# Optimization experiments

Hardware: AMD Instinct MI355X
Metric: run time of the kernel (lower is better)

Reference implementation:

```python
import jax, jax.numpy as jnp
import numpy as np

B, N, D = 64, 197, 768
H, HD = 12, 64
MAX_REL = 14
SCALE = HD ** -0.5


def rel_indices(n, max_rel):
    """Static 2D relative-position index matrices of shape (n, n), int32."""
    lq = n - 1
    side = int(lq ** 0.5)
    r = np.arange(lq)
    dv = r[None, :] // side - r[:, None] // side
    dh = r[None, :] % side - r[:, None] % side
    fv = np.clip(dv, -max_rel, max_rel) + max_rel + 1
    fh = np.clip(dh, -max_rel, max_rel) + max_rel + 1
    # pad one row/col of zeros on top-left for the cls token (index 0)
    fv = np.pad(fv, ((1, 0), (1, 0)), constant_values=0)
    fh = np.pad(fh, ((1, 0), (1, 0)), constant_values=0)
    return fv.astype(np.int32), fh.astype(np.int32)


IDX_V, IDX_H = rel_indices(N, MAX_REL)


def setup_inputs() -> dict:
    key = jax.random.key(0)
    ks = jax.random.split(key, 13)
    lin = lambda k: jax.random.normal(k, (D, H * HD), jnp.float32) * 0.02
    tab = lambda k: jax.random.normal(k, (2 * MAX_REL + 2, HD), jnp.float32) * 0.02
    return {
        'x': jax.random.normal(ks[0], (B, N, D), jnp.float32),
        'wq': lin(ks[1]), 'bq': jnp.zeros((H * HD,), jnp.float32),
        'wk': lin(ks[2]), 'bk': jnp.zeros((H * HD,), jnp.float32),
        'wv': lin(ks[3]), 'bv': jnp.zeros((H * HD,), jnp.float32),
        'wp': jax.random.normal(ks[4], (H * HD, D), jnp.float32) * 0.02,
        'bp': jnp.zeros((D,), jnp.float32),
        'rel_k_v': tab(ks[5]), 'rel_k_h': tab(ks[6]),
        'rel_v_v': tab(ks[7]), 'rel_v_h': tab(ks[8]),
    }


def reference(x, wq, bq, wk, bk, wv, bv, wp, bp, rel_k_v, rel_k_h, rel_v_v, rel_v_h):
    b, n, _ = x.shape
    # qkv projections -> (B, H, N, HD)
    q = (x @ wq + bq).reshape(b, n, H, HD).transpose(0, 2, 1, 3)
    k = (x @ wk + bk).reshape(b, n, H, HD).transpose(0, 2, 1, 3)
    v = (x @ wv + bv).reshape(b, n, H, HD).transpose(0, 2, 1, 3)

    attn = jnp.einsum('bhid,bhjd->bhij', q, k) * SCALE
    # iRPE key bias: gather (N, N, HD) table then contract with q per query pos
    r_p_k = rel_k_v[IDX_V] + rel_k_h[IDX_H]              # (N, N, HD)
    attn = attn + jnp.einsum('bhid,ijd->bhij', q, r_p_k) * SCALE
    attn = jax.nn.softmax(attn, axis=-1)

    out = jnp.einsum('bhij,bhjd->bhid', attn, v)
    # iRPE value bias
    r_p_v = rel_v_v[IDX_V] + rel_v_h[IDX_H]              # (N, N, HD)
    out = out + jnp.einsum('bhij,ijd->bhid', attn, r_p_v)

    out = out.transpose(0, 2, 1, 3).reshape(b, n, H * HD)
    return out @ wp + bp
```

## Files before the change

kernel.cpp:

```cpp
#include <hip/hip_runtime.h>
#include <math.h>

#define SCALE_ 0.125f

typedef unsigned short u16;
typedef __attribute__((ext_vector_type(8))) _Float16 half8;
typedef __attribute__((ext_vector_type(4))) float f32x4;
#define MFMA_H __builtin_amdgcn_mfma_f32_16x16x32_f16

__device__ __forceinline__ u16 f2h(float f) {
    union { _Float16 h; u16 u; } v; v.h = (_Float16)f; return v.u;
}
__device__ __forceinline__ float h2f(u16 u) {
    union { _Float16 h; u16 u; } v; v.u = u; return (float)v.h;
}
__device__ __forceinline__ void gload16(const u16* g, u16* l) {
    __builtin_amdgcn_global_load_lds(
        (const __attribute__((address_space(1))) void*)g,
        (__attribute__((address_space(3))) void*)l, 16, 0, 0);
}
__device__ __forceinline__ half8 ld_h8(const u16* p) {
    return *(const half8*)p;
}

__global__ void prep_half_x(const float* __restrict__ x, u16* __restrict__ xh) {
    size_t idx = ((size_t)blockIdx.x * 256 + threadIdx.x) * 8;
    float4 a = *(const float4*)(x + idx), b = *(const float4*)(x + idx + 4);
    float f[8] = {a.x, a.y, a.z, a.w, b.x, b.y, b.z, b.w};
    u16 hs[8];
    #pragma unroll
    for (int e = 0; e < 8; ++e) hs[e] = f2h(f[e]);
    *(uint4*)(xh + idx) = *(uint4*)hs;
}

__global__ void prep_w(const float* __restrict__ w0, const float* __restrict__ w1,
                       const float* __restrict__ w2, const float* __restrict__ w3,
                       u16* o0, u16* o1, u16* o2, u16* o3) {
    const float* W; u16* oh;
    if (blockIdx.z == 0)      { W = w0; oh = o0; }
    else if (blockIdx.z == 1) { W = w1; oh = o1; }
    else if (blockIdx.z == 2) { W = w2; oh = o2; }
    else                      { W = w3; oh = o3; }

    __shared__ float t[64 * 68];
    int k0 = blockIdx.y * 64, n0 = blockIdx.x * 64;
    int tid = threadIdx.x;
    #pragma unroll
    for (int rr = 0; rr < 4; ++rr) {
        int r = (tid >> 4) + rr * 16;
        int c = (tid & 15) * 4;
        *(float4*)&t[r * 68 + c] = *(const float4*)(W + (size_t)(k0 + r) * 768 + n0 + c);
    }
    __syncthreads();
    int n = tid >> 2, kc = (tid & 3) * 16;
    u16 hs[16];
    #pragma unroll
    for (int e = 0; e < 16; ++e) hs[e] = f2h(t[(kc + e) * 68 + n]);
    size_t o = (size_t)(n0 + n) * 768 + k0 + kc;
    *(uint4*)(oh + o) = *(uint4*)hs;
    *(uint4*)(oh + o + 8) = *(uint4*)(hs + 8);
}

__global__ void prep_tabs(const float* __restrict__ rkv, const float* __restrict__ rkh,
                          const float* __restrict__ rvv, const float* __restrict__ rvh,
                          u16* tk, u16* rth) {
    for (int idx = threadIdx.x; idx < 4096; idx += 256) {
        int r = idx >> 6, d = idx & 63;
        float tv = 0.f;
        if (r < 30) tv = rkv[r * 64 + d];
        else if (r >= 32 && r < 62) tv = rkh[(r - 32) * 64 + d];
        tk[idx] = f2h(tv);
        int dd = idx >> 6, rr = idx & 63;
        float vv = 0.f;
        if (rr < 30) vv = rvv[rr * 64 + dd];
        else if (rr >= 32 && rr < 62) vv = rvh[(rr - 32) * 64 + dd];
        rth[idx] = f2h(vv);
    }
}

__global__ void prep_vt(const u16* __restrict__ rth, u16* __restrict__ vtp) {
    u16* vb = vtp + (size_t)blockIdx.x * 64 * 288;
    for (int t = threadIdx.x; t < 64 * 91; t += 256) {
        int d = t / 91;
        int c = 197 + (t - d * 91);
        u16 val = 0;
        if (c >= 208 && c < 272) val = rth[d * 64 + (c - 208)];
        vb[d * 288 + c] = val;
    }
}

__global__ __launch_bounds__(256) void vtrans(const u16* __restrict__ v,
                                              u16* __restrict__ vt) {
    __shared__ u16 L[64 * 72];
    const int bh = blockIdx.x;
    const u16* src = v + (size_t)bh * 197 * 64;
    u16* dst = vt + (size_t)bh * 64 * 288;
    const int tid = threadIdx.x;
    const int keyl = tid >> 2;
    const int c8 = (tid & 3) * 16;
    for (int k0 = 0; k0 < 197; k0 += 64) {
        __syncthreads();
        int key = k0 + keyl;
        if (key < 197) {
            uint4 g0 = *(const uint4*)(src + key * 64 + c8);
            uint4 g1 = *(const uint4*)(src + key * 64 + c8 + 8);
            u16 t0[8]; *(uint4*)t0 = g0;
            u16 t1[8]; *(uint4*)t1 = g1;
            #pragma unroll
            for (int e = 0; e < 8; ++e) L[(c8 + e) * 72 + keyl] = t0[e];
            #pragma unroll
            for (int e = 0; e < 8; ++e) L[(c8 + 8 + e) * 72 + keyl] = t1[e];
        }
        __syncthreads();
        int d = tid >> 2, cc = (tid & 3) * 16;
        if (k0 + cc < 197) {
            int nvalid = min(16, 197 - k0 - cc);
            if (nvalid == 16) {
                *(uint4*)(dst + d * 288 + k0 + cc)     = *(const uint4*)&L[d * 72 + cc];
                *(uint4*)(dst + d * 288 + k0 + cc + 8) = *(const uint4*)&L[d * 72 + cc + 8];
            } else {
                for (int e = 0; e < nvalid; ++e)
                    dst[d * 288 + k0 + cc + e] = L[d * 72 + cc + e];
            }
        }
    }
}

__global__ __launch_bounds__(256, 4) void gemm_f16(
    const u16* __restrict__ Ah,
    const u16* __restrict__ B0, const u16* __restrict__ B1, const u16* __restrict__ B2,
    const float* __restrict__ bias0, const float* __restrict__ bias1,
    const float* __restrict__ bias2,
    u16* qo, u16* ko, u16* vo, float* outf, int nz, int kind)
{
    __shared__ u16 SM[128 * 64 * 2];
    u16* As = SM;
    u16* Bs = SM + 128 * 64;

    const int p = blockIdx.x;
    const int xcd = p & 7, s = p >> 3;
    const int mcnt = (xcd < 3) ? 13 : 12;
    const int mbase = (xcd < 3) ? xcd * 13 : 39 + (xcd - 3) * 12;
    const int jn = 6 * nz;
    if (s >= mcnt * jn) return;
    const int mb = mbase + s / jn;
    const int j = s % jn;
    const int z = j / 6;
    const int nb = j % 6;

    const u16* Bt = B0; const float* bias = bias0;
    if (z == 1) { Bt = B1; bias = bias1; }
    else if (z == 2) { Bt = B2; bias = bias2; }

    const int m0 = mb * 128, n0 = nb * 128;
    const int tid = threadIdx.x;
    const int w = tid >> 6, lane = tid & 63, quad = lane >> 4, l16 = lane & 15;
    const int wm = (w >> 1) * 64, wn = (w & 1) * 64;
    const int rl8 = lane >> 3, cs = lane & 7;
    const int csrc = (cs ^ rl8) * 8;

    f32x4 acc[4][4];
    #pragma unroll
    for (int a = 0; a < 4; ++a)
        #pragma unroll
        for (int b = 0; b < 4; ++b) acc[a][b] = (f32x4){0, 0, 0, 0};

    for (int kt = 0; kt < 768; kt += 64) {
        __syncthreads();
        #pragma unroll
        for (int i = 0; i < 4; ++i) {
            int r = w * 32 + i * 8 + rl8;
            int arow = min(m0 + r, 12607);
            gload16(Ah + (size_t)arow * 768 + kt + csrc, &As[(w * 32 + i * 8) * 64]);
            gload16(Bt + (size_t)(n0 + r) * 768 + kt + csrc, &Bs[(w * 32 + i * 8) * 64]);
        }
        __syncthreads();
        #pragma unroll
        for (int kb = 0; kb < 2; ++kb) {
            const int slot = ((kb * 4 + quad) ^ (l16 & 7)) * 8;
            half8 ah[4], bf[4];
            #pragma unroll
            for (int mi = 0; mi < 4; ++mi) {
                ah[mi] = ld_h8(&As[(wm + mi * 16 + l16) * 64 + slot]);
                bf[mi] = ld_h8(&Bs[(wn + mi * 16 + l16) * 64 + slot]);
            }
            #pragma unroll
            for (int ni = 0; ni < 4; ++ni)
                #pragma unroll
                for (int mi = 0; mi < 4; ++mi)
                    acc[mi][ni] = MFMA_H(ah[mi], bf[ni], acc[mi][ni], 0, 0, 0);
        }
    }

    if (kind == 1) {
        #pragma unroll
        for (int mi = 0; mi < 4; ++mi) {
            #pragma unroll
            for (int r = 0; r < 4; ++r) {
                int gr = m0 + wm + mi * 16 + quad * 4 + r;
                if (gr >= 12608) continue;
                #pragma unroll
                for (int ni = 0; ni < 4; ++ni) {
                    int gc = n0 + wn + ni * 16 + l16;
                    outf[(size_t)gr * 768 + gc] = acc[mi][ni][r] + bias[gc];
                }
            }
        }
        return;
    }

    __syncthreads();
    u16* Cs = SM;
    #pragma unroll
    for (int mi = 0; mi < 4; ++mi) {
        #pragma unroll
        for (int ni = 0; ni < 4; ++ni) {
            int col = wn + ni * 16 + l16;
            float bv = bias[n0 + col];
            #pragma unroll
            for (int r = 0; r < 4; ++r)
                Cs[(wm + mi * 16 + quad * 4 + r) * 128 + col] = f2h(acc[mi][ni][r] + bv);
        }
    }
    __syncthreads();
    u16* O = (z == 0) ? qo : ((z == 1) ? ko : vo);
    int row = tid >> 1, halfc = tid & 1;
    int gr = m0 + row;
    if (gr < 12608) {
        int bb = gr / 197, ii = gr - bb * 197;
        int h = (n0 >> 6) + halfc;
        u16* dst = O + ((size_t)(bb * 12 + h) * 197 + ii) * 64;
        const u16* src = &Cs[row * 128 + halfc * 64];
        #pragma unroll
        for (int e = 0; e < 8; ++e)
            *(uint4*)(dst + e * 8) = *(const uint4*)(src + e * 8);
    }
}

__global__ __launch_bounds__(512, 4) void attn_mfma(
    const u16* __restrict__ qh, const u16* __restrict__ kh,
    const u16* __restrict__ tk, const u16* __restrict__ vt,
    u16* __restrict__ oh)
{
    __shared__ u16 Ph[64 * 296];
    __shared__ float Tvh[64 * 68];
    __shared__ float red[64 * 4];

    const int p = blockIdx.x;
    const int xcd = p & 7, s = p >> 3;
    const int bh = xcd * 96 + (s >> 2);
    const int qt = s & 3;
    const int I0 = qt * 64;
    const int tid = threadIdx.x;
    const int w = tid >> 6, lane = tid & 63, quad = lane >> 4, l16 = lane & 15;
    const int mf = w >> 1, nh = w & 1;
    const int mr0 = mf * 16;
    const size_t base = (size_t)bh * 197 * 64;
    const uint4 z4 = make_uint4(0, 0, 0, 0);

    half8 qa[2];
    {
        int i = I0 + mr0 + l16;
        bool ok = i < 197;
        const u16* qp = qh + base + (size_t)i * 64 + quad * 8;
        #pragma unroll
        for (int kb = 0; kb < 2; ++kb) {
            uint4 a = ok ? *(const uint4*)(qp + kb * 32) : z4;
            *(uint4*)&qa[kb] = a;
        }
    }

    #pragma unroll
    for (int s2 = 0; s2 < 2; ++s2) {
        int c = (nh * 2 + s2) * 16 + l16;
        f32x4 acc = (f32x4){0, 0, 0, 0};
        #pragma unroll
        for (int kb = 0; kb < 2; ++kb) {
            half8 th = ld_h8(tk + c * 64 + kb * 32 + quad * 8);
            acc = MFMA_H(qa[kb], th, acc, 0, 0, 0);
        }
        #pragma unroll
        for (int r = 0; r < 4; ++r)
            Tvh[(mr0 + quad * 4 + r) * 68 + c] = acc[r];
    }

    f32x4 sacc[7];
    #pragma unroll
    for (int s1 = 0; s1 < 7; ++s1) sacc[s1] = (f32x4){0, 0, 0, 0};
    #pragma unroll
    for (int s1 = 0; s1 < 7; ++s1) {
        int j = (nh * 7 + s1) * 16 + l16;
        bool ok = j < 197;
        const u16* kp = kh + base + (size_t)j * 64 + quad * 8;
        f32x4 c = sacc[s1];
        #pragma unroll
        for (int kb = 0; kb < 2; ++kb) {
            uint4 a = ok ? *(const uint4*)(kp + kb * 32) : z4;
            half8 kf; *(uint4*)&kf = a;
            c = MFMA_H(qa[kb], kf, c, 0, 0, 0);
        }
        sacc[s1] = c;
    }
    __syncthreads();

    float sval[7][4];
    int jj[7];
    #pragma unroll
    for (int s1 = 0; s1 < 7; ++s1) jj[s1] = (nh * 7 + s1) * 16 + l16;
    int ivA[4], ihA[4], iA[4];
    #pragma unroll
    for (int r = 0; r < 4; ++r) {
        int i = I0 + mr0 + quad * 4 + r;
        int qi = i - 1;
        int iv = qi / 14;
        ivA[r] = iv; ihA[r] = qi - iv * 14; iA[r] = i;
    }
    #pragma unroll
    for (int s1 = 0; s1 < 7; ++s1) {
        int j = jj[s1];
        if (j < 197) {
            int kj = j - 1;
            int jv = kj / 14;
            int jh2 = kj - jv * 14;
            #pragma unroll
            for (int r = 0; r < 4; ++r) {
                int m = mr0 + quad * 4 + r;
                int fv = 0, fh = 0;
                if (iA[r] > 0 && j > 0) {
                    int dv = jv - ivA[r]; dv = min(14, max(-14, dv));
                    int dh = jh2 - ihA[r]; dh = min(14, max(-14, dh));
                    fv = dv + 15; fh = dh + 15;
                }
                sval[s1][r] = (sacc[s1][r] + Tvh[m * 68 + fv] + Tvh[m * 68 + 32 + fh]) * SCALE_;
            }
        } else {
            #pragma unroll
            for (int r = 0; r < 4; ++r) sval[s1][r] = -1e30f;
        }
    }

    #pragma unroll
    for (int r = 0; r < 4; ++r) {
        float mx = sval[0][r];
        #pragma unroll
        for (int s1 = 1; s1 < 7; ++s1) mx = fmaxf(mx, sval[s1][r]);
        #pragma unroll
        for (int off = 1; off < 16; off <<= 1) mx = fmaxf(mx, __shfl_xor(mx, off, 64));
        if (l16 == 0) red[(mr0 + quad * 4 + r) * 4 + nh] = mx;
    }
    __syncthreads();

    #pragma unroll
    for (int r = 0; r < 4; ++r) {
        int m = mr0 + quad * 4 + r;
        float M = fmaxf(red[m * 4], red[m * 4 + 1]);
        float sum = 0.f;
        #pragma unroll
        for (int s1 = 0; s1 < 7; ++s1) {
            float pv = (jj[s1] < 197) ? __expf(sval[s1][r] - M) : 0.f;
            sval[s1][r] = pv;
            sum += pv;
        }
        #pragma unroll
        for (int off = 1; off < 16; off <<= 1) sum += __shfl_xor(sum, off, 64);
        if (l16 == 0) red[m * 4 + 2 + nh] = sum;
    }
    #pragma unroll
    for (int s1 = 0; s1 < 7; ++s1) {
        int j = jj[s1];
        if (j < 208) {
            #pragma unroll
            for (int r = 0; r < 4; ++r)
                Ph[(mr0 + quad * 4 + r) * 296 + j] = f2h(sval[s1][r]);
        }
    }
    __syncthreads();

    for (int q8 = 0; q8 < 8; ++q8) {
        int m = w * 8 + q8;
        int i = I0 + m;
        float bs = 0.f;
        if (lane < 14) {
            #pragma unroll
            for (int c = 0; c < 14; ++c) bs += h2f(Ph[m * 296 + 1 + lane * 14 + c]);
        } else if (lane >= 16 && lane < 30) {
            int c = lane - 16;
            #pragma unroll
            for (int b = 0; b < 14; ++b) bs += h2f(Ph[m * 296 + 1 + b * 14 + c]);
        }
        float pcls = h2f(Ph[m * 296]);
        float val;
        if (i == 0) {
            float lsum = red[m * 4 + 2] + red[m * 4 + 3];
            val = ((lane & 31) == 0) ? lsum : 0.f;
        } else {
            int qi = i - 1;
            int iv = qi / 14, ih = qi - (qi / 14) * 14;
            int r = lane & 31;
            int bidx = (lane < 32) ? (r + iv - 15) : (r + ih - 15);
            bool ok = (bidx >= 0) && (bidx <= 13) && (r < 30);
            int src = (lane < 32) ? min(13, max(0, bidx)) : 16 + min(13, max(0, bidx));
            float g = __shfl(bs, src, 64);
            val = ok ? g : 0.f;
            if (r == 0) val += pcls;
        }
        int col = (lane < 32) ? (208 + lane) : (240 + (lane - 32));
        Ph[m * 296 + col] = f2h(val);
    }
    for (int t = tid; t < 64 * 16; t += 512)
        Ph[(t >> 4) * 296 + 272 + (t & 15)] = 0;
    __syncthreads();

    {
        f32x4 oacc[2] = {(f32x4){0, 0, 0, 0}, (f32x4){0, 0, 0, 0}};
        const u16* vb = vt + (size_t)bh * 64 * 288;
        #pragma unroll
        for (int ks = 0; ks < 9; ++ks) {
            half8 ap = ld_h8(&Ph[(mr0 + l16) * 296 + ks * 32 + quad * 8]);
            #pragma unroll
            for (int sd = 0; sd < 2; ++sd) {
                int d = (nh * 2 + sd) * 16 + l16;
                half8 bv = ld_h8(vb + (size_t)d * 288 + ks * 32 + quad * 8);
                oacc[sd] = MFMA_H(ap, bv, oacc[sd], 0, 0, 0);
            }
        }
        int b = bh / 12, h = bh - b * 12;
        float rl[4];
        #pragma unroll
        for (int r = 0; r < 4; ++r) {
            int m = mr0 + quad * 4 + r;
            rl[r] = 1.f / (red[m * 4 + 2] + red[m * 4 + 3]);
        }
        #pragma unroll
        for (int sd = 0; sd < 2; ++sd) {
            int d = (nh * 2 + sd) * 16 + l16;
            #pragma unroll
            for (int r = 0; r < 4; ++r) {
                int i = I0 + mr0 + quad * 4 + r;
                if (i < 197) {
                    oh[((size_t)(b * 197 + i)) * 768 + h * 64 + d] =
                        f2h(oacc[sd][r] * rl[r]);
                }
            }
        }
    }
}

extern "C" void kernel_launch(void* const* d_in, const int* in_sizes, int n_in,
                              void* d_out, int out_size, void* d_ws, size_t ws_size,
                              hipStream_t stream)
{
    const float* x   = (const float*)d_in[0];
    const float* wq  = (const float*)d_in[1];
    const float* bq  = (const float*)d_in[2];
    const float* wk  = (const float*)d_in[3];
    const float* bk  = (const float*)d_in[4];
    const float* wv  = (const float*)d_in[5];
    const float* bv  = (const float*)d_in[6];
    const float* wp  = (const float*)d_in[7];
    const float* bp  = (const float*)d_in[8];
    const float* rkv = (const float*)d_in[9];
    const float* rkh = (const float*)d_in[10];
    const float* rvv = (const float*)d_in[11];
    const float* rvh = (const float*)d_in[12];
    float* out = (float*)d_out;

    const size_t SZX = (size_t)12608 * 768;
    const size_t SZW = (size_t)768 * 768;
    const size_t SZVT = (size_t)768 * 64 * 288;

    u16* xh  = (u16*)d_ws;
    u16* qh_ = xh + SZX;
    u16* kh_ = qh_ + SZX;
    u16* vh_ = kh_ + SZX;
    u16* vt  = vh_ + SZX;
    u16* wt  = vt + SZVT;
    u16* wqh = wt;
    u16* wkh = wt + SZW;
    u16* wvh = wt + 2 * SZW;
    u16* wph = wt + 3 * SZW;
    u16* tk  = wt + 4 * SZW;
    u16* rth = tk + 4096;
    u16* oh_ = xh;

    prep_half_x<<<4728, 256, 0, stream>>>(x, xh);
    prep_w<<<dim3(12, 12, 4), 256, 0, stream>>>(wq, wk, wv, wp, wqh, wkh, wvh, wph);
    prep_tabs<<<1, 256, 0, stream>>>(rkv, rkh, rvv, rvh, tk, rth);
    prep_vt<<<768, 256, 0, stream>>>(rth, vt);

    gemm_f16<<<1872, 256, 0, stream>>>(
        xh, wqh, wkh, wvh, bq, bk, bv, qh_, kh_, vh_, nullptr, 3, 0);

    vtrans<<<768, 256, 0, stream>>>(vh_, vt);

    attn_mfma<<<3072, 512, 0, stream>>>(qh_, kh_, tk, vt, oh_);

    gemm_f16<<<624, 256, 0, stream>>>(
        oh_, wph, wph, wph, bp, bp, bp, nullptr, nullptr, nullptr, out, 1, 1);
}
```

Before: 350.6 us.

## Compute iRPE value-bias bucket sums via MFMA with one-hot matrix, shrink LDS

Replaces the per-row scalar LDS loops that sum attention probabilities into row and column buckets with an MFMA against a precomputed one-hot grouping matrix. The results go into a smaller shared buffer. The key-bias table Tvh is stored as fp16 and aliased into that buffer, and the clamp on the relative indices is dropped because the 14x14 grid never exceeds the range. Less LDS per block allows raising launch bounds to 6 blocks per CU, which improves occupancy. The costs are lower precision in the bias table, an extra global read of the one-hot matrix, and more register pressure under the tighter bounds.

```diff
diff --git a/kernel.cpp b/kernel.cpp
--- a/kernel.cpp
+++ b/kernel.cpp
@@ -63,7 +63,7 @@
 
 __global__ void prep_tabs(const float* __restrict__ rkv, const float* __restrict__ rkh,
                           const float* __restrict__ rvv, const float* __restrict__ rvh,
-                          u16* tk, u16* rth) {
+                          u16* tk, u16* rth, u16* gt) {
     for (int idx = threadIdx.x; idx < 4096; idx += 256) {
         int r = idx >> 6, d = idx & 63;
         float tv = 0.f;
@@ -75,6 +75,17 @@
         if (rr < 30) vv = rvv[rr * 64 + dd];
         else if (rr >= 32 && rr < 62) vv = rvh[(rr - 32) * 64 + dd];
         rth[idx] = f2h(vv);
+    }
+    for (int idx = threadIdx.x; idx < 32 * 224; idx += 256) {
+        int g = idx / 224, j = idx - (idx / 224) * 224;
+        float v = 0.f;
+        if (j >= 1 && j < 197) {
+            int jq = j - 1;
+            int jv = jq / 14, jh = jq - jv * 14;
+            if (g < 14) v = (jv == g) ? 1.f : 0.f;
+            else if (g >= 16 && g < 30) v = (jh == g - 16) ? 1.f : 0.f;
+        }
+        gt[idx] = f2h(v);
     }
 }
 
@@ -237,14 +248,16 @@
     }
 }
 
-__global__ __launch_bounds__(512, 4) void attn_mfma(
+__global__ __launch_bounds__(512, 6) void attn_mfma(
     const u16* __restrict__ qh, const u16* __restrict__ kh,
     const u16* __restrict__ tk, const u16* __restrict__ vt,
+    const u16* __restrict__ gt,
     u16* __restrict__ oh)
 {
     __shared__ u16 Ph[64 * 296];
-    __shared__ float Tvh[64 * 68];
+    __shared__ float BsT[64 * 36];
     __shared__ float red[64 * 4];
+    u16* Tvh16 = (u16*)BsT;
 
     const int p = blockIdx.x;
     const int xcd = p & 7, s = p >> 3;
@@ -281,7 +294,7 @@
         }
         #pragma unroll
         for (int r = 0; r < 4; ++r)
-            Tvh[(mr0 + quad * 4 + r) * 68 + c] = acc[r];
+            Tvh16[(mr0 + quad * 4 + r) * 68 + c] = f2h(acc[r]);
     }
 
     f32x4 sacc[7];
@@ -327,11 +340,11 @@
                 int m = mr0 + quad * 4 + r;
                 int fv = 0, fh = 0;
                 if (iA[r] > 0 && j > 0) {
-                    int dv = jv - ivA[r]; dv = min(14, max(-14, dv));
-                    int dh = jh2 - ihA[r]; dh = min(14, max(-14, dh));
-                    fv = dv + 15; fh = dh + 15;
+                    fv = jv - ivA[r] + 15;
+                    fh = jh2 - ihA[r] + 15;
                 }
-                sval[s1][r] = (sacc[s1][r] + Tvh[m * 68 + fv] + Tvh[m * 68 + 32 + fh]) * SCALE_;
+                sval[s1][r] = (sacc[s1][r] + h2f(Tvh16[m * 68 + fv])
+                                         + h2f(Tvh16[m * 68 + 32 + fh])) * SCALE_;
             }
         } else {
             #pragma unroll
@@ -374,41 +387,49 @@
                 Ph[(mr0 + quad * 4 + r) * 296 + j] = f2h(sval[s1][r]);
         }
     }
-    __syncthreads();
-
-    for (int q8 = 0; q8 < 8; ++q8) {
-        int m = w * 8 + q8;
+    #pragma unroll
+    for (int t = 0; t < 2; ++t) {
+        int ii2 = tid + t * 512;
+        Ph[(ii2 >> 4) * 296 + 208 + (ii2 & 15)] = 0;
+    }
+    __syncthreads();
+
+    {
+        f32x4 bacc = (f32x4){0, 0, 0, 0};
+        #pragma unroll
+        for (int ks = 0; ks < 7; ++ks) {
+            half8 ap = ld_h8(&Ph[(mr0 + l16) * 296 + ks * 32 + quad * 8]);
+            half8 gp = ld_h8(gt + (nh * 16 + l16) * 224 + ks * 32 + quad * 8);
+            bacc = MFMA_H(ap, gp, bacc, 0, 0, 0);
+        }
+        #pragma unroll
+        for (int r = 0; r < 4; ++r)
+            BsT[(mr0 + quad * 4 + r) * 36 + nh * 16 + l16] = bacc[r];
+    }
+    for (int t = tid; t < 64 * 16; t += 512)
+        Ph[(t >> 4) * 296 + 272 + (t & 15)] = 0;
+    __syncthreads();
+
+    #pragma unroll
+    for (int t = 0; t < 8; ++t) {
+        int idx = tid + t * 512;
+        int m = idx >> 6, c = idx & 63;
         int i = I0 + m;
-        float bs = 0.f;
-        if (lane < 14) {
-            #pragma unroll
-            for (int c = 0; c < 14; ++c) bs += h2f(Ph[m * 296 + 1 + lane * 14 + c]);
-        } else if (lane >= 16 && lane < 30) {
-            int c = lane - 16;
-            #pragma unroll
-            for (int b = 0; b < 14; ++b) bs += h2f(Ph[m * 296 + 1 + b * 14 + c]);
-        }
-        float pcls = h2f(Ph[m * 296]);
         float val;
         if (i == 0) {
-            float lsum = red[m * 4 + 2] + red[m * 4 + 3];
-            val = ((lane & 31) == 0) ? lsum : 0.f;
+            val = (c == 0 || c == 32) ? (red[m * 4 + 2] + red[m * 4 + 3]) : 0.f;
         } else {
             int qi = i - 1;
             int iv = qi / 14, ih = qi - (qi / 14) * 14;
-            int r = lane & 31;
-            int bidx = (lane < 32) ? (r + iv - 15) : (r + ih - 15);
+            int r = c & 31;
+            int bidx = r + ((c < 32) ? iv : ih) - 15;
             bool ok = (bidx >= 0) && (bidx <= 13) && (r < 30);
-            int src = (lane < 32) ? min(13, max(0, bidx)) : 16 + min(13, max(0, bidx));
-            float g = __shfl(bs, src, 64);
-            val = ok ? g : 0.f;
-            if (r == 0) val += pcls;
-        }
-        int col = (lane < 32) ? (208 + lane) : (240 + (lane - 32));
-        Ph[m * 296 + col] = f2h(val);
-    }
-    for (int t = tid; t < 64 * 16; t += 512)
-        Ph[(t >> 4) * 296 + 272 + (t & 15)] = 0;
+            int src = ((c < 32) ? 0 : 16) + min(13, max(0, bidx));
+            val = ok ? BsT[m * 36 + src] : 0.f;
+            if (r == 0) val += h2f(Ph[m * 296]);
+        }
+        Ph[m * 296 + 208 + c] = f2h(val);
+    }
     __syncthreads();
 
     {
@@ -481,11 +502,12 @@
     u16* wph = wt + 3 * SZW;
     u16* tk  = wt + 4 * SZW;
     u16* rth = tk + 4096;
+    u16* gt  = rth + 4096;
     u16* oh_ = xh;
 
     prep_half_x<<<4728, 256, 0, stream>>>(x, xh);
     prep_w<<<dim3(12, 12, 4), 256, 0, stream>>>(wq, wk, wv, wp, wqh, wkh, wvh, wph);
-    prep_tabs<<<1, 256, 0, stream>>>(rkv, rkh, rvv, rvh, tk, rth);
+    prep_tabs<<<1, 256, 0, stream>>>(rkv, rkh, rvv, rvh, tk, rth, gt);
     prep_vt<<<768, 256, 0, stream>>>(rth, vt);
 
     gemm_f16<<<1872, 256, 0, stream>>>(
@@ -493,7 +515,7 @@
 
     vtrans<<<768, 256, 0, stream>>>(vh_, vt);
 
-    attn_mfma<<<3072, 512, 0, stream>>>(qh_, kh_, tk, vt, oh_);
+    attn_mfma<<<3072, 512, 0, stream>>>(qh_, kh_, tk, vt, gt, oh_);
 
     gemm_f16<<<624, 256, 0, stream>>>(
         oh_, wph, wph, wph, bp, bp, bp, nullptr, nullptr, nullptr, out, 1, 1);
```

Measured after the change: 367.3 us. +4.8%, slower.
